# Kernel tuning notes

Measured on AMD Instinct MI355X. Metric: run time of the kernel, lower is better.

The kernel has to match this reference:

```python
import jax, jax.numpy as jnp
import numpy as np


def setup_inputs() -> dict:
    key = jax.random.key(0)
    ks = jax.random.split(key, 6)
    B, H, W, C = 4, 64, 64, 256
    D = 256  # d_model
    s = 0.02
    return {
        "features": jax.random.normal(ks[0], (B, H, W, C), dtype=jnp.float32),
        "Wq": jax.random.normal(ks[1], (C, D), dtype=jnp.float32) * s,
        "bq": jnp.zeros((D,), dtype=jnp.float32),
        "Wk": jax.random.normal(ks[2], (C, D), dtype=jnp.float32) * s,
        "bk": jnp.zeros((D,), dtype=jnp.float32),
        "Wv": jax.random.normal(ks[3], (C, D), dtype=jnp.float32) * s,
        "bv": jnp.zeros((D,), dtype=jnp.float32),
        "Wo": jax.random.normal(ks[4], (D, C), dtype=jnp.float32) * s,
        "bo": jnp.zeros((C,), dtype=jnp.float32),
    }


def reference(features, Wq, bq, Wk, bk, Wv, bv, Wo, bo):
    # features: [B, H, W, C] (NHWC). 1x1 convs are per-pixel GEMMs, so flatten
    # spatial dims to N = H*W tokens and do single-head self-attention.
    B, H, W, C = features.shape
    D = Wq.shape[1]
    x = features.reshape(B, H * W, C)          # [B, N, C]
    q = x @ Wq + bq                            # [B, N, D]
    k = x @ Wk + bk                            # [B, N, D]
    v = x @ Wv + bv                            # [B, N, D]
    scale = np.float32(1.0 / np.sqrt(D))
    scores = jnp.einsum("bnd,bmd->bnm", q, k) * scale   # [B, N, N]
    attn = jax.nn.softmax(scores, axis=-1)               # [B, N, N]
    out = jnp.einsum("bnm,bmd->bnd", attn, v)            # [B, N, D]
    out = out @ Wo + bo                                  # [B, N, C]
    return out.reshape(B, H, W, C)
```

## Files before the change

kernel.cpp:

```cpp
#include <hip/hip_runtime.h>
#include <hip/hip_bf16.h>


typedef __attribute__((ext_vector_type(8))) short short8;
typedef __attribute__((ext_vector_type(4))) short short4v;
typedef __attribute__((ext_vector_type(4))) float floatx4;

#define NB 4
#define NT 4096
#define CD 256
#define MTOT (NB * NT)

__device__ __forceinline__ short bf16s(float f) {
    union { float f; unsigned u; } a; a.f = f;
    unsigned u = a.u;
    return (short)((u + 0x7fffu + ((u >> 16) & 1u)) >> 16);
}

__device__ __forceinline__ float bf2f(short s) {
    union { unsigned u; float f; } a;
    a.u = ((unsigned)(unsigned short)s) << 16;
    return a.f;
}

__device__ __forceinline__ short8 ld8(const short* p) {
    return *(const short8*)p;
}

__device__ __forceinline__ floatx4 mfma16(short8 a, short8 b, floatx4 c) {
    return __builtin_amdgcn_mfma_f32_16x16x32_bf16(a, b, c, 0, 0, 0);
}

__device__ __forceinline__ void dma16(const void* g, void* l) {
    __builtin_amdgcn_global_load_lds(
        (const __attribute__((address_space(1))) void*)g,
        (__attribute__((address_space(3))) void*)l, 16, 0, 0);
}

__global__ __launch_bounds__(256) void k_convx(const float* __restrict__ x,
                                               short* __restrict__ xb) {
    int i = (blockIdx.x * 256 + threadIdx.x) * 4;
    float4 v = *(const float4*)(x + i);
    short4v o;
    o.x = bf16s(v.x); o.y = bf16s(v.y); o.z = bf16s(v.z); o.w = bf16s(v.w);
    *(short4v*)(xb + i) = o;
}

__global__ __launch_bounds__(256) void k_convw(const float* __restrict__ w0,
                                               const float* __restrict__ w1,
                                               const float* __restrict__ w2,
                                               const float* __restrict__ w3,
                                               short* __restrict__ wt) {
    int z = blockIdx.y;
    const float* w = (z == 0) ? w0 : (z == 1) ? w1 : (z == 2) ? w2 : w3;
    int c = blockIdx.x;
    int n = threadIdx.x;
    wt[z * 65536 + n * 256 + c] = bf16s(w[c * 256 + n]);
}

__global__ __launch_bounds__(256) void k_proj3(const short* __restrict__ A,
                                               const short* __restrict__ Wt,
                                               const float* __restrict__ bq,
                                               const float* __restrict__ bk,
                                               const float* __restrict__ bv,
                                               short* __restrict__ Qb,
                                               short* __restrict__ Kb,
                                               short* __restrict__ Vt) {
    __shared__ __align__(16) short Ws[16384];
    int z = blockIdx.z;
    const short* W = Wt + z * 65536;
    const float* bias = (z == 0) ? bq : (z == 1) ? bk : bv;
    float scale = (z == 0) ? 0.0625f : 1.0f;
    int m0 = blockIdx.x * 128;
    int n0 = blockIdx.y * 64;
    int tid = threadIdx.x;
    int w = tid >> 6, l = tid & 63, r = l & 15, q = l >> 4;

#pragma unroll
    for (int cg = 0; cg < 8; ++cg)
        dma16(W + (size_t)(n0 + w * 16 + r) * CD + (cg * 4 + q) * 8,
              &Ws[w * 4096 + cg * 512]);
    __syncthreads();

    const short* a0 = A + (size_t)(m0 + w * 32 + r) * CD;
    const short* a1 = a0 + 16 * CD;
    floatx4 acc[2][4];
#pragma unroll
    for (int rt = 0; rt < 2; ++rt)
#pragma unroll
        for (int j = 0; j < 4; ++j) acc[rt][j] = (floatx4){0.f, 0.f, 0.f, 0.f};
#pragma unroll
    for (int c = 0; c < 8; ++c) {
        short8 af0 = ld8(a0 + c * 32 + q * 8);
        short8 af1 = ld8(a1 + c * 32 + q * 8);
#pragma unroll
        for (int j = 0; j < 4; ++j) {
            short8 wf = ld8(&Ws[j * 4096 + c * 512 + l * 8]);
            acc[0][j] = mfma16(af0, wf, acc[0][j]);
            acc[1][j] = mfma16(af1, wf, acc[1][j]);
        }
    }
#pragma unroll
    for (int rt = 0; rt < 2; ++rt)
#pragma unroll
        for (int j = 0; j < 4; ++j) {
            int col = n0 + j * 16 + r;
            float bvv = bias[col];
#pragma unroll
            for (int i = 0; i < 4; ++i) {
                int row = m0 + w * 32 + rt * 16 + q * 4 + i;
                short s = bf16s((acc[rt][j][i] + bvv) * scale);
                if (z == 0) Qb[(size_t)row * CD + col] = s;
                else if (z == 1) Kb[(size_t)row * CD + col] = s;
                else {
                    int bb = row >> 12, lm = row & (NT - 1);
                    Vt[((size_t)bb * CD + col) * NT + lm] = s;
                }
            }
        }
}

__global__ __launch_bounds__(256, 3) void k_attn(const short* __restrict__ Qb,
                                                 const short* __restrict__ Kb,
                                                 const short* __restrict__ Vt,
                                                 short* __restrict__ Op0,
                                                 short* __restrict__ Op1,
                                                 short* __restrict__ Op2,
                                                 float* __restrict__ Lp,
                                                 int nks) {
    __shared__ __align__(16) short Ks[2][8192];
    __shared__ __align__(16) short P[64][36];

    const int tid = threadIdx.x;
    const int w = tid >> 6;
    const int l = tid & 63;
    const int r = l & 15, q = l >> 4;
    const int b = blockIdx.y;
    const int ks = blockIdx.z;
    const int m0 = blockIdx.x * 64;
    const int qq = 128 / nks, rem = 128 % nks;
    const int u0 = ks * qq + (ks < rem ? ks : rem);
    const int cnt = qq + (ks < rem ? 1 : 0);
    const int t0 = u0 * 32;
    const int tt_d = w & 1;
    const int cb_d = (w >> 1) * 4;
    const short* Qp = Qb + (size_t)b * NT * CD;
    const short* Kp = Kb + (size_t)b * NT * CD;
    const short* Vp = Vt + (size_t)b * CD * NT;
    short* Op = (ks == 0) ? Op0 : (ks == 1) ? Op1 : Op2;

    short8 qf[8];
#pragma unroll
    for (int c = 0; c < 8; ++c)
        qf[c] = ld8(Qp + (size_t)(m0 + w * 16 + r) * CD + c * 32 + q * 8);

    floatx4 o[4][4];
#pragma unroll
    for (int rt = 0; rt < 4; ++rt)
#pragma unroll
        for (int dt = 0; dt < 4; ++dt) o[rt][dt] = (floatx4){0.f, 0.f, 0.f, 0.f};
    float ls = 0.f;

#pragma unroll
    for (int j = 0; j < 4; ++j)
        dma16(Kp + (size_t)(t0 + tt_d * 16 + r) * CD + ((cb_d + j) * 4 + q) * 8,
              &Ks[0][tt_d * 4096 + (cb_d + j) * 512]);

#pragma unroll 1
    for (int it = 0; it < cnt; ++it) {
        const int p = it & 1;
        const int n0 = t0 + it * 32;
        __syncthreads();

        short8 vf[4];
#pragma unroll
        for (int dt = 0; dt < 4; ++dt)
            vf[dt] = ld8(Vp + (size_t)(w * 64 + dt * 16 + r) * NT + n0 + q * 8);

        if (it + 1 < cnt) {
#pragma unroll
            for (int j = 0; j < 4; ++j)
                dma16(Kp + (size_t)(n0 + 32 + tt_d * 16 + r) * CD + ((cb_d + j) * 4 + q) * 8,
                      &Ks[1 - p][tt_d * 4096 + (cb_d + j) * 512]);
        }

        floatx4 s0 = {0.f, 0.f, 0.f, 0.f};
        floatx4 s1 = {0.f, 0.f, 0.f, 0.f};
#pragma unroll
        for (int c = 0; c < 8; ++c) {
            s0 = mfma16(ld8(&Ks[p][c * 512 + l * 8]), qf[c], s0);
            s1 = mfma16(ld8(&Ks[p][4096 + c * 512 + l * 8]), qf[c], s1);
        }

#pragma unroll
        for (int tt = 0; tt < 2; ++tt) {
            floatx4 sv = tt ? s1 : s0;
            float e0 = __expf(sv[0]), e1 = __expf(sv[1]);
            float e2 = __expf(sv[2]), e3 = __expf(sv[3]);
            ls += (e0 + e1) + (e2 + e3);
            short4v pk;
            pk.x = bf16s(e0); pk.y = bf16s(e1); pk.z = bf16s(e2); pk.w = bf16s(e3);
            *(short4v*)&P[w * 16 + r][tt * 16 + q * 4] = pk;
        }
        asm volatile("s_waitcnt lgkmcnt(0)\n\ts_barrier" ::: "memory");

#pragma unroll
        for (int rt = 0; rt < 4; ++rt) {
            short8 pf = ld8(&P[rt * 16 + r][q * 8]);
#pragma unroll
            for (int dt = 0; dt < 4; ++dt)
                o[rt][dt] = mfma16(pf, vf[dt], o[rt][dt]);
        }
    }

    ls += __shfl_xor(ls, 16);
    ls += __shfl_xor(ls, 32);
    if (l < 16)
        Lp[(size_t)ks * MTOT + b * NT + m0 + w * 16 + l] = ls;

#pragma unroll
    for (int rt = 0; rt < 4; ++rt)
#pragma unroll
        for (int i = 0; i < 4; ++i) {
            int row = m0 + rt * 16 + q * 4 + i;
#pragma unroll
            for (int dt = 0; dt < 4; ++dt)
                Op[((size_t)b * NT + row) * CD + w * 64 + dt * 16 + r] =
                    bf16s(o[rt][dt][i]);
        }
}

__global__ __launch_bounds__(256) void k_oproj(const short* __restrict__ Op0,
                                               const short* __restrict__ Op1,
                                               const short* __restrict__ Op2,
                                               const float* __restrict__ Lp,
                                               const short* __restrict__ Wot,
                                               const float* __restrict__ bo,
                                               float* __restrict__ out, int nks) {
    __shared__ __align__(16) short Ws[16384];
    int m0 = blockIdx.x * 128;
    int n0 = blockIdx.y * 64;
    int tid = threadIdx.x;
    int w = tid >> 6, l = tid & 63, r = l & 15, q = l >> 4;

#pragma unroll
    for (int cg = 0; cg < 8; ++cg)
        dma16(Wot + (size_t)(n0 + w * 16 + r) * CD + (cg * 4 + q) * 8,
              &Ws[w * 4096 + cg * 512]);
    __syncthreads();

    int row0 = m0 + w * 32 + r;
    float lt0 = Lp[row0] + Lp[MTOT + row0];
    float lt1 = Lp[row0 + 16] + Lp[MTOT + row0 + 16];
    if (nks == 3) { lt0 += Lp[2 * MTOT + row0]; lt1 += Lp[2 * MTOT + row0 + 16]; }
    float inv0 = 1.0f / lt0, inv1 = 1.0f / lt1;
    const short* p00 = Op0 + (size_t)row0 * CD;
    const short* p01 = Op1 + (size_t)row0 * CD;
    const short* p02 = Op2 + (size_t)row0 * CD;
    floatx4 acc[2][4];
#pragma unroll
    for (int rt = 0; rt < 2; ++rt)
#pragma unroll
        for (int j = 0; j < 4; ++j) acc[rt][j] = (floatx4){0.f, 0.f, 0.f, 0.f};
#pragma unroll
    for (int c = 0; c < 8; ++c) {
        int off0 = c * 32 + q * 8, off1 = 16 * CD + c * 32 + q * 8;
        short8 x0 = ld8(p00 + off0), y0 = ld8(p01 + off0);
        short8 x1 = ld8(p00 + off1), y1 = ld8(p01 + off1);
        short8 af0, af1;
        if (nks == 3) {
            short8 z0 = ld8(p02 + off0), z1 = ld8(p02 + off1);
#pragma unroll
            for (int jj = 0; jj < 8; ++jj) {
                af0[jj] = bf16s((bf2f(x0[jj]) + bf2f(y0[jj]) + bf2f(z0[jj])) * inv0);
                af1[jj] = bf16s((bf2f(x1[jj]) + bf2f(y1[jj]) + bf2f(z1[jj])) * inv1);
            }
        } else {
#pragma unroll
            for (int jj = 0; jj < 8; ++jj) {
                af0[jj] = bf16s((bf2f(x0[jj]) + bf2f(y0[jj])) * inv0);
                af1[jj] = bf16s((bf2f(x1[jj]) + bf2f(y1[jj])) * inv1);
            }
        }
#pragma unroll
        for (int j = 0; j < 4; ++j) {
            short8 wf = ld8(&Ws[j * 4096 + c * 512 + l * 8]);
            acc[0][j] = mfma16(af0, wf, acc[0][j]);
            acc[1][j] = mfma16(af1, wf, acc[1][j]);
        }
    }
#pragma unroll
    for (int rt = 0; rt < 2; ++rt)
#pragma unroll
        for (int j = 0; j < 4; ++j) {
            int col = n0 + j * 16 + r;
            float bvv = bo[col];
#pragma unroll
            for (int i = 0; i < 4; ++i)
                out[(size_t)(m0 + w * 32 + rt * 16 + q * 4 + i) * CD + col] =
                    acc[rt][j][i] + bvv;
        }
}

extern "C" void kernel_launch(void* const* d_in, const int* in_sizes, int n_in,
                              void* d_out, int out_size, void* d_ws, size_t ws_size,
                              hipStream_t stream) {
    const float* x  = (const float*)d_in[0];
    const float* Wq = (const float*)d_in[1];
    const float* bq = (const float*)d_in[2];
    const float* Wk = (const float*)d_in[3];
    const float* bk = (const float*)d_in[4];
    const float* Wv = (const float*)d_in[5];
    const float* bv = (const float*)d_in[6];
    const float* Wo = (const float*)d_in[7];
    const float* bo = (const float*)d_in[8];
    float* out = (float*)d_out;

    char* ws = (char*)d_ws;
    const size_t MB = 1024u * 1024u;
    short* xb  = (short*)(ws);
    short* Op0 = (short*)(ws);
    short* Qb  = (short*)(ws + 8 * MB);
    short* Kb  = (short*)(ws + 16 * MB);
    short* Vt  = (short*)(ws + 24 * MB);
    short* Op1 = (short*)(ws + 32 * MB);
    short* Wt  = (short*)(ws + 40 * MB);
    float* Lp  = (float*)(ws + 40 * MB + 512 * 1024);
    short* Op2 = (short*)(ws + 41 * MB);

    int nks = (ws_size >= 49 * MB + 512 * 1024) ? 3 : 2;
    if (nks == 2) Op2 = Op1;

    k_convx<<<dim3(MTOT * CD / (256 * 4)), 256, 0, stream>>>(x, xb);
    k_convw<<<dim3(256, 4), 256, 0, stream>>>(Wq, Wk, Wv, Wo, Wt);
    k_proj3<<<dim3(MTOT / 128, CD / 64, 3), 256, 0, stream>>>(xb, Wt, bq, bk, bv, Qb, Kb, Vt);
    k_attn<<<dim3(NT / 64, NB, nks), 256, 0, stream>>>(Qb, Kb, Vt, Op0, Op1, Op2, Lp, nks);
    k_oproj<<<dim3(MTOT / 128, CD / 64), 256, 0, stream>>>(Op0, Op1, Op2, Lp, Wt + 196608, bo, out, nks);
}
```

Baseline: 258.7 us.

## Widen attention blocks to 512 threads with 64-key tiles and fixed 2-way split

The attention kernel now runs 8 waves per block. Four row groups times two key halves compute the score tiles for 64 keys per step, and each wave accumulates P·V for a 32-wide slice of the head dimension. This halves the per-wave output accumulators and doubles the key tile per barrier. The key-split is fixed at 2, with four partial softmax-denominator rows, so the three-way split path and its workspace-size check are removed. Exponentials are packed to bf16 with the hardware v_cvt_pk_bf16_f32 instruction instead of manual rounding, and the larger LDS footprint may limit how many blocks fit per CU.

New measurement: 287.7 us. 1.11x slower.

```diff
diff --git a/kernel.cpp b/kernel.cpp
--- a/kernel.cpp
+++ b/kernel.cpp
@@ -120,45 +120,42 @@
         }
 }
 
-__global__ __launch_bounds__(256, 3) void k_attn(const short* __restrict__ Qb,
+__global__ __launch_bounds__(512, 4) void k_attn(const short* __restrict__ Qb,
                                                  const short* __restrict__ Kb,
                                                  const short* __restrict__ Vt,
                                                  short* __restrict__ Op0,
                                                  short* __restrict__ Op1,
-                                                 short* __restrict__ Op2,
-                                                 float* __restrict__ Lp,
-                                                 int nks) {
-    __shared__ __align__(16) short Ks[2][8192];
-    __shared__ __align__(16) short P[64][36];
+                                                 float* __restrict__ Lp) {
+    __shared__ __align__(16) short Ks[2][16384];
+    __shared__ __align__(16) short P[64][68];
 
     const int tid = threadIdx.x;
     const int w = tid >> 6;
     const int l = tid & 63;
     const int r = l & 15, q = l >> 4;
+    const int rg = w & 3;
+    const int th = w >> 2;
     const int b = blockIdx.y;
     const int ks = blockIdx.z;
     const int m0 = blockIdx.x * 64;
-    const int qq = 128 / nks, rem = 128 % nks;
-    const int u0 = ks * qq + (ks < rem ? ks : rem);
-    const int cnt = qq + (ks < rem ? 1 : 0);
-    const int t0 = u0 * 32;
-    const int tt_d = w & 1;
-    const int cb_d = (w >> 1) * 4;
+    const int t0 = ks * 2048;
+    const int tt_d = w & 3;
+    const int cb_d = (w >> 2) * 4;
     const short* Qp = Qb + (size_t)b * NT * CD;
     const short* Kp = Kb + (size_t)b * NT * CD;
     const short* Vp = Vt + (size_t)b * CD * NT;
-    short* Op = (ks == 0) ? Op0 : (ks == 1) ? Op1 : Op2;
+    short* Op = (ks == 0) ? Op0 : Op1;
 
     short8 qf[8];
 #pragma unroll
     for (int c = 0; c < 8; ++c)
-        qf[c] = ld8(Qp + (size_t)(m0 + w * 16 + r) * CD + c * 32 + q * 8);
-
-    floatx4 o[4][4];
+        qf[c] = ld8(Qp + (size_t)(m0 + rg * 16 + r) * CD + c * 32 + q * 8);
+
+    floatx4 o[4][2];
 #pragma unroll
     for (int rt = 0; rt < 4; ++rt)
 #pragma unroll
-        for (int dt = 0; dt < 4; ++dt) o[rt][dt] = (floatx4){0.f, 0.f, 0.f, 0.f};
+        for (int dt = 0; dt < 2; ++dt) o[rt][dt] = (floatx4){0.f, 0.f, 0.f, 0.f};
     float ls = 0.f;
 
 #pragma unroll
@@ -167,20 +164,23 @@
               &Ks[0][tt_d * 4096 + (cb_d + j) * 512]);
 
 #pragma unroll 1
-    for (int it = 0; it < cnt; ++it) {
+    for (int it = 0; it < 32; ++it) {
         const int p = it & 1;
-        const int n0 = t0 + it * 32;
+        const int n0 = t0 + it * 64;
         __syncthreads();
 
-        short8 vf[4];
-#pragma unroll
-        for (int dt = 0; dt < 4; ++dt)
-            vf[dt] = ld8(Vp + (size_t)(w * 64 + dt * 16 + r) * NT + n0 + q * 8);
-
-        if (it + 1 < cnt) {
+        short8 vf[2][2];
+#pragma unroll
+        for (int t2 = 0; t2 < 2; ++t2)
+#pragma unroll
+            for (int dt = 0; dt < 2; ++dt)
+                vf[t2][dt] = ld8(Vp + (size_t)(w * 32 + dt * 16 + r) * NT +
+                                 n0 + t2 * 32 + q * 8);
+
+        if (it + 1 < 32) {
 #pragma unroll
             for (int j = 0; j < 4; ++j)
-                dma16(Kp + (size_t)(n0 + 32 + tt_d * 16 + r) * CD + ((cb_d + j) * 4 + q) * 8,
+                dma16(Kp + (size_t)(n0 + 64 + tt_d * 16 + r) * CD + ((cb_d + j) * 4 + q) * 8,
                       &Ks[1 - p][tt_d * 4096 + (cb_d + j) * 512]);
         }
 
@@ -188,8 +188,8 @@
         floatx4 s1 = {0.f, 0.f, 0.f, 0.f};
 #pragma unroll
         for (int c = 0; c < 8; ++c) {
-            s0 = mfma16(ld8(&Ks[p][c * 512 + l * 8]), qf[c], s0);
-            s1 = mfma16(ld8(&Ks[p][4096 + c * 512 + l * 8]), qf[c], s1);
+            s0 = mfma16(ld8(&Ks[p][(th * 2 + 0) * 4096 + c * 512 + l * 8]), qf[c], s0);
+            s1 = mfma16(ld8(&Ks[p][(th * 2 + 1) * 4096 + c * 512 + l * 8]), qf[c], s1);
         }
 
 #pragma unroll
@@ -198,25 +198,29 @@
             float e0 = __expf(sv[0]), e1 = __expf(sv[1]);
             float e2 = __expf(sv[2]), e3 = __expf(sv[3]);
             ls += (e0 + e1) + (e2 + e3);
-            short4v pk;
-            pk.x = bf16s(e0); pk.y = bf16s(e1); pk.z = bf16s(e2); pk.w = bf16s(e3);
-            *(short4v*)&P[w * 16 + r][tt * 16 + q * 4] = pk;
+            unsigned pk01, pk23;
+            asm("v_cvt_pk_bf16_f32 %0, %1, %2" : "=v"(pk01) : "v"(e0), "v"(e1));
+            asm("v_cvt_pk_bf16_f32 %0, %1, %2" : "=v"(pk23) : "v"(e2), "v"(e3));
+            uint2 pk; pk.x = pk01; pk.y = pk23;
+            *(uint2*)&P[rg * 16 + r][th * 32 + tt * 16 + q * 4] = pk;
         }
         asm volatile("s_waitcnt lgkmcnt(0)\n\ts_barrier" ::: "memory");
 
 #pragma unroll
         for (int rt = 0; rt < 4; ++rt) {
-            short8 pf = ld8(&P[rt * 16 + r][q * 8]);
-#pragma unroll
-            for (int dt = 0; dt < 4; ++dt)
-                o[rt][dt] = mfma16(pf, vf[dt], o[rt][dt]);
+#pragma unroll
+            for (int t2 = 0; t2 < 2; ++t2) {
+                short8 pf = ld8(&P[rt * 16 + r][t2 * 32 + q * 8]);
+                o[rt][0] = mfma16(pf, vf[t2][0], o[rt][0]);
+                o[rt][1] = mfma16(pf, vf[t2][1], o[rt][1]);
+            }
         }
     }
 
     ls += __shfl_xor(ls, 16);
     ls += __shfl_xor(ls, 32);
     if (l < 16)
-        Lp[(size_t)ks * MTOT + b * NT + m0 + w * 16 + l] = ls;
+        Lp[(size_t)(ks * 2 + th) * MTOT + b * NT + m0 + rg * 16 + l] = ls;
 
 #pragma unroll
     for (int rt = 0; rt < 4; ++rt)
@@ -224,19 +228,18 @@
         for (int i = 0; i < 4; ++i) {
             int row = m0 + rt * 16 + q * 4 + i;
 #pragma unroll
-            for (int dt = 0; dt < 4; ++dt)
-                Op[((size_t)b * NT + row) * CD + w * 64 + dt * 16 + r] =
+            for (int dt = 0; dt < 2; ++dt)
+                Op[((size_t)b * NT + row) * CD + w * 32 + dt * 16 + r] =
                     bf16s(o[rt][dt][i]);
         }
 }
 
 __global__ __launch_bounds__(256) void k_oproj(const short* __restrict__ Op0,
                                                const short* __restrict__ Op1,
-                                               const short* __restrict__ Op2,
                                                const float* __restrict__ Lp,
                                                const short* __restrict__ Wot,
                                                const float* __restrict__ bo,
-                                               float* __restrict__ out, int nks) {
+                                               float* __restrict__ out) {
     __shared__ __align__(16) short Ws[16384];
     int m0 = blockIdx.x * 128;
     int n0 = blockIdx.y * 64;
@@ -250,13 +253,13 @@
     __syncthreads();
 
     int row0 = m0 + w * 32 + r;
-    float lt0 = Lp[row0] + Lp[MTOT + row0];
-    float lt1 = Lp[row0 + 16] + Lp[MTOT + row0 + 16];
-    if (nks == 3) { lt0 += Lp[2 * MTOT + row0]; lt1 += Lp[2 * MTOT + row0 + 16]; }
+    float lt0 = (Lp[row0] + Lp[MTOT + row0]) +
+                (Lp[2 * MTOT + row0] + Lp[3 * MTOT + row0]);
+    float lt1 = (Lp[row0 + 16] + Lp[MTOT + row0 + 16]) +
+                (Lp[2 * MTOT + row0 + 16] + Lp[3 * MTOT + row0 + 16]);
     float inv0 = 1.0f / lt0, inv1 = 1.0f / lt1;
     const short* p00 = Op0 + (size_t)row0 * CD;
     const short* p01 = Op1 + (size_t)row0 * CD;
-    const short* p02 = Op2 + (size_t)row0 * CD;
     floatx4 acc[2][4];
 #pragma unroll
     for (int rt = 0; rt < 2; ++rt)
@@ -268,19 +271,10 @@
         short8 x0 = ld8(p00 + off0), y0 = ld8(p01 + off0);
         short8 x1 = ld8(p00 + off1), y1 = ld8(p01 + off1);
         short8 af0, af1;
-        if (nks == 3) {
-            short8 z0 = ld8(p02 + off0), z1 = ld8(p02 + off1);
-#pragma unroll
-            for (int jj = 0; jj < 8; ++jj) {
-                af0[jj] = bf16s((bf2f(x0[jj]) + bf2f(y0[jj]) + bf2f(z0[jj])) * inv0);
-                af1[jj] = bf16s((bf2f(x1[jj]) + bf2f(y1[jj]) + bf2f(z1[jj])) * inv1);
-            }
-        } else {
-#pragma unroll
-            for (int jj = 0; jj < 8; ++jj) {
-                af0[jj] = bf16s((bf2f(x0[jj]) + bf2f(y0[jj])) * inv0);
-                af1[jj] = bf16s((bf2f(x1[jj]) + bf2f(y1[jj])) * inv1);
-            }
+#pragma unroll
+        for (int jj = 0; jj < 8; ++jj) {
+            af0[jj] = bf16s((bf2f(x0[jj]) + bf2f(y0[jj])) * inv0);
+            af1[jj] = bf16s((bf2f(x1[jj]) + bf2f(y1[jj])) * inv1);
         }
 #pragma unroll
         for (int j = 0; j < 4; ++j) {
@@ -326,14 +320,10 @@
     short* Op1 = (short*)(ws + 32 * MB);
     short* Wt  = (short*)(ws + 40 * MB);
     float* Lp  = (float*)(ws + 40 * MB + 512 * 1024);
-    short* Op2 = (short*)(ws + 41 * MB);
-
-    int nks = (ws_size >= 49 * MB + 512 * 1024) ? 3 : 2;
-    if (nks == 2) Op2 = Op1;
 
     k_convx<<<dim3(MTOT * CD / (256 * 4)), 256, 0, stream>>>(x, xb);
     k_convw<<<dim3(256, 4), 256, 0, stream>>>(Wq, Wk, Wv, Wo, Wt);
     k_proj3<<<dim3(MTOT / 128, CD / 64, 3), 256, 0, stream>>>(xb, Wt, bq, bk, bv, Qb, Kb, Vt);
-    k_attn<<<dim3(NT / 64, NB, nks), 256, 0, stream>>>(Qb, Kb, Vt, Op0, Op1, Op2, Lp, nks);
-    k_oproj<<<dim3(MTOT / 128, CD / 64), 256, 0, stream>>>(Op0, Op1, Op2, Lp, Wt + 196608, bo, out, nks);
-}
+    k_attn<<<dim3(NT / 64, NB, 2), 512, 0, stream>>>(Qb, Kb, Vt, Op0, Op1, Lp);
+    k_oproj<<<dim3(MTOT / 128, CD / 64), 256, 0, stream>>>(Op0, Op1, Lp, Wt + 196608, bo, out);
+}
```

## Stage K tiles through registers, double-buffer P, drop one barrier per iteration

Applied to the files above, without the earlier changes.

Replaces the direct global-to-LDS DMA for K tiles with register loads issued at the top of the iteration and stored into the alternate LDS buffer after the softmax step. The P buffer is double-buffered so the leading __syncthreads can be removed, leaving one barrier per key tile. It also switches the bf16 packing to the hardware v_cvt_pk_bf16_f32 instruction. The register staging costs 16 extra VGPRs per thread, which may hurt occupancy under launch_bounds(256,3), and the hardware conversion may round differently from the manual bf16 routine.

Measured after the change: 259.8 us. Within noise of the previous version (+0.4%).

```diff
diff --git a/kernel.cpp b/kernel.cpp
--- a/kernel.cpp
+++ b/kernel.cpp
@@ -129,7 +129,7 @@
                                                  float* __restrict__ Lp,
                                                  int nks) {
     __shared__ __align__(16) short Ks[2][8192];
-    __shared__ __align__(16) short P[64][36];
+    __shared__ __align__(16) short P[2][64][36];
 
     const int tid = threadIdx.x;
     const int w = tid >> 6;
@@ -161,28 +161,31 @@
         for (int dt = 0; dt < 4; ++dt) o[rt][dt] = (floatx4){0.f, 0.f, 0.f, 0.f};
     float ls = 0.f;
 
+    short8 kst[4];
 #pragma unroll
     for (int j = 0; j < 4; ++j)
-        dma16(Kp + (size_t)(t0 + tt_d * 16 + r) * CD + ((cb_d + j) * 4 + q) * 8,
-              &Ks[0][tt_d * 4096 + (cb_d + j) * 512]);
+        kst[j] = ld8(Kp + (size_t)(t0 + tt_d * 16 + r) * CD + ((cb_d + j) * 4 + q) * 8);
+#pragma unroll
+    for (int j = 0; j < 4; ++j)
+        *(short8*)&Ks[0][tt_d * 4096 + (cb_d + j) * 512 + l * 8] = kst[j];
+    asm volatile("s_waitcnt lgkmcnt(0)\n\ts_barrier" ::: "memory");
 
 #pragma unroll 1
     for (int it = 0; it < cnt; ++it) {
         const int p = it & 1;
         const int n0 = t0 + it * 32;
-        __syncthreads();
+
+        if (it + 1 < cnt) {
+#pragma unroll
+            for (int j = 0; j < 4; ++j)
+                kst[j] = ld8(Kp + (size_t)(n0 + 32 + tt_d * 16 + r) * CD +
+                             ((cb_d + j) * 4 + q) * 8);
+        }
 
         short8 vf[4];
 #pragma unroll
         for (int dt = 0; dt < 4; ++dt)
             vf[dt] = ld8(Vp + (size_t)(w * 64 + dt * 16 + r) * NT + n0 + q * 8);
-
-        if (it + 1 < cnt) {
-#pragma unroll
-            for (int j = 0; j < 4; ++j)
-                dma16(Kp + (size_t)(n0 + 32 + tt_d * 16 + r) * CD + ((cb_d + j) * 4 + q) * 8,
-                      &Ks[1 - p][tt_d * 4096 + (cb_d + j) * 512]);
-        }
 
         floatx4 s0 = {0.f, 0.f, 0.f, 0.f};
         floatx4 s1 = {0.f, 0.f, 0.f, 0.f};
@@ -198,15 +201,24 @@
             float e0 = __expf(sv[0]), e1 = __expf(sv[1]);
             float e2 = __expf(sv[2]), e3 = __expf(sv[3]);
             ls += (e0 + e1) + (e2 + e3);
-            short4v pk;
-            pk.x = bf16s(e0); pk.y = bf16s(e1); pk.z = bf16s(e2); pk.w = bf16s(e3);
-            *(short4v*)&P[w * 16 + r][tt * 16 + q * 4] = pk;
-        }
+            unsigned pk01, pk23;
+            asm("v_cvt_pk_bf16_f32 %0, %1, %2" : "=v"(pk01) : "v"(e0), "v"(e1));
+            asm("v_cvt_pk_bf16_f32 %0, %1, %2" : "=v"(pk23) : "v"(e2), "v"(e3));
+            uint2 pk; pk.x = pk01; pk.y = pk23;
+            *(uint2*)&P[p][w * 16 + r][tt * 16 + q * 4] = pk;
+        }
+
+        if (it + 1 < cnt) {
+#pragma unroll
+            for (int j = 0; j < 4; ++j)
+                *(short8*)&Ks[1 - p][tt_d * 4096 + (cb_d + j) * 512 + l * 8] = kst[j];
+        }
+
         asm volatile("s_waitcnt lgkmcnt(0)\n\ts_barrier" ::: "memory");
 
 #pragma unroll
         for (int rt = 0; rt < 4; ++rt) {
-            short8 pf = ld8(&P[rt * 16 + r][q * 8]);
+            short8 pf = ld8(&P[p][rt * 16 + r][q * 8]);
 #pragma unroll
             for (int dt = 0; dt < 4; ++dt)
                 o[rt][dt] = mfma16(pf, vf[dt], o[rt][dt]);
```
